# Kernel optimization log

Hardware: AMD Instinct MI355X
Metric: run time of the kernel (lower is better)

Reference implementation:

```python
import jax, jax.numpy as jnp
import numpy as np
import math

C = 512          # in_planes
H = 8            # num_heads
D = C // H       # head_dim = 64
EPS = 1e-12      # torch F.normalize eps


def _l2norm(x):
    # F.normalize(x, dim=-1): x / max(||x||_2, eps)
    n = jnp.sqrt(jnp.sum(x * x, axis=-1, keepdims=True))
    return x / jnp.maximum(n, EPS)


def setup_inputs() -> dict:
    key = jax.random.key(0)
    ks = jax.random.split(key, 8)
    q = jax.random.normal(ks[0], (8, 8, 256, C), dtype=jnp.float32)
    kv = jax.random.normal(ks[1], (8, 8, 512, C), dtype=jnp.float32)
    s = 0.02
    Wq = jax.random.normal(ks[2], (C, C), dtype=jnp.float32) * s
    bq = jax.random.normal(ks[3], (C,), dtype=jnp.float32) * s
    Wkv = jax.random.normal(ks[4], (2 * C, C), dtype=jnp.float32) * s
    bkv = jax.random.normal(ks[5], (2 * C,), dtype=jnp.float32) * s
    Wm = jax.random.normal(ks[6], (C, C), dtype=jnp.float32) * s
    bm = jax.random.normal(ks[7], (C,), dtype=jnp.float32) * s
    return {"q": q, "kv": kv, "Wq": Wq, "bq": bq, "Wkv": Wkv, "bkv": bkv, "Wm": Wm, "bm": bm}


def reference(q, kv, Wq, bq, Wkv, bkv, Wm, bm):
    b, t, lq, c = q.shape
    lk = kv.shape[2]
    shortcut = q

    # Q projection -> (b,t,h,lq,d), L2-normalized over d
    qh = (q @ Wq.T + bq).reshape(b, t, lq, H, D)
    qh = _l2norm(jnp.moveaxis(qh, 3, 2))  # (b,t,h,lq,d)

    # KV projection -> (b,t,2h,lk,d); first H heads = k, last H = v
    kvh = (kv @ Wkv.T + bkv).reshape(b, t, lk, 2 * H, D)
    kvh = jnp.moveaxis(kvh, 3, 2)          # (b,t,2h,lk,d)
    kh = _l2norm(kvh[:, :, :H])            # (b,t,h,lk,d)
    vh = _l2norm(kvh[:, :, H:])            # (b,t,h,lk,d)

    # cosine attention
    att = jnp.einsum('bthqd,bthkd->bthqk', qh, kh) / math.sqrt(D)
    att = jax.nn.softmax(att, axis=-1)
    x = jnp.einsum('bthqk,bthkd->bthqd', att, vh)  # (b,t,h,lq,d)

    # merge heads, output projection, residual
    x = jnp.moveaxis(x, 2, 3).reshape(b, t, lq, c)
    return x @ Wm.T + bm + shortcut
```

## Files before the change

### kernel.cpp

```cpp
#include <hip/hip_runtime.h>
#include <hip/hip_bf16.h>

using bf = __bf16;
typedef __attribute__((ext_vector_type(8))) __bf16 bf16x8;
typedef __attribute__((ext_vector_type(4))) float f32x4;

#define MFMA(a, b, c) __builtin_amdgcn_mfma_f32_16x16x32_bf16((a), (b), (c), 0, 0, 0)
#define GLL16(g, s)                                                         \
    __builtin_amdgcn_global_load_lds(                                       \
        (const __attribute__((address_space(1))) void*)(g),                 \
        (__attribute__((address_space(3))) void*)(s), 16, 0, 0)

static __device__ __forceinline__ void cvt_one(const float* __restrict__ s,
                                               bf* __restrict__ d, int i)
{
    const f32x4 a = ((const f32x4*)s)[2 * i];
    const f32x4 b = ((const f32x4*)s)[2 * i + 1];
    bf16x8 r;
#pragma unroll
    for (int k = 0; k < 4; ++k) { r[k] = (bf)a[k]; r[4 + k] = (bf)b[k]; }
    ((bf16x8*)d)[i] = r;
}

__global__ __launch_bounds__(256) void cvt2(const float* __restrict__ s1, bf* __restrict__ d1, int n1,
                                            const float* __restrict__ s2, bf* __restrict__ d2, int n2)
{
    int i = blockIdx.x * 256 + threadIdx.x;
    if (i < n1) { cvt_one(s1, d1, i); return; }
    i -= n1;
    if (i < n2) cvt_one(s2, d2, i);
}

__global__ __launch_bounds__(256) void cvt3(const float* __restrict__ s1, bf* __restrict__ d1, int n1,
                                            const float* __restrict__ s2, bf* __restrict__ d2, int n2,
                                            const float* __restrict__ s3, bf* __restrict__ d3, int n3)
{
    int i = blockIdx.x * 256 + threadIdx.x;
    if (i < n1) { cvt_one(s1, d1, i); return; }
    i -= n1;
    if (i < n2) { cvt_one(s2, d2, i); return; }
    i -= n2;
    if (i < n3) cvt_one(s3, d3, i);
}

template <int EPI>
__global__ __launch_bounds__(256) void gemm128(
    const bf* __restrict__ A, const bf* __restrict__ W,
    const float* __restrict__ bias, const float* __restrict__ res,
    void* __restrict__ Cout, int M, int N, int K)
{
    __shared__ __attribute__((aligned(16))) bf As[128 * 32];
    __shared__ __attribute__((aligned(16))) bf Bs[128 * 32];

    const int lane = threadIdx.x & 63;
    const int wave = threadIdx.x >> 6;
    const int lm = lane & 15;
    const int quad = lane >> 4;
    const int row0 = blockIdx.x * 128, col0 = blockIdx.y * 128;
    const int wrow = (wave >> 1) * 64, wcol = (wave & 1) * 64;

    const int sr = lane >> 2;
    const int sc = (lane & 3) * 8;
    const bf* Ag = A + (size_t)(row0 + wave * 32 + sr) * K + sc;
    const bf* Wg = W + (size_t)(col0 + wave * 32 + sr) * K + sc;
    bf* AsW = As + wave * 1024;
    bf* BsW = Bs + wave * 1024;

    f32x4 acc[4][4] = {};

    for (int k0 = 0; k0 < K; k0 += 32) {
        GLL16(Ag + k0, AsW);
        GLL16(Ag + (size_t)16 * K + k0, AsW + 512);
        GLL16(Wg + k0, BsW);
        GLL16(Wg + (size_t)16 * K + k0, BsW + 512);
        __syncthreads();

        bf16x8 a[4], b[4];
#pragma unroll
        for (int i = 0; i < 4; ++i)
            a[i] = *(const bf16x8*)(As + (wrow + i * 16 + lm) * 32 + quad * 8);
#pragma unroll
        for (int j = 0; j < 4; ++j)
            b[j] = *(const bf16x8*)(Bs + (wcol + j * 16 + lm) * 32 + quad * 8);
#pragma unroll
        for (int i = 0; i < 4; ++i)
#pragma unroll
            for (int j = 0; j < 4; ++j)
                acc[i][j] = MFMA(a[i], b[j], acc[i][j]);
        __syncthreads();
    }

    float bv[4];
#pragma unroll
    for (int j = 0; j < 4; ++j) bv[j] = bias[col0 + wcol + j * 16 + lm];

    if (EPI == 0) {
        bf* C = (bf*)Cout;
#pragma unroll
        for (int i = 0; i < 4; ++i) {
#pragma unroll
            for (int r = 0; r < 4; ++r) {
                float v[4];
                float ss = 0.f;
#pragma unroll
                for (int j = 0; j < 4; ++j) {
                    const float x = acc[i][j][r] + bv[j];
                    v[j] = x;
                    ss += x * x;
                }
                ss += __shfl_xor(ss, 1, 64);
                ss += __shfl_xor(ss, 2, 64);
                ss += __shfl_xor(ss, 4, 64);
                ss += __shfl_xor(ss, 8, 64);
                const float inv = 1.0f / fmaxf(sqrtf(ss), 1e-12f);
                const int row = row0 + wrow + i * 16 + quad * 4 + r;
#pragma unroll
                for (int j = 0; j < 4; ++j)
                    C[(size_t)row * N + col0 + wcol + j * 16 + lm] = (bf)(v[j] * inv);
            }
        }
    } else {
        float* C = (float*)Cout;
#pragma unroll
        for (int i = 0; i < 4; ++i) {
#pragma unroll
            for (int r = 0; r < 4; ++r) {
                const int row = row0 + wrow + i * 16 + quad * 4 + r;
#pragma unroll
                for (int j = 0; j < 4; ++j) {
                    const size_t idx = (size_t)row * N + col0 + wcol + j * 16 + lm;
                    C[idx] = acc[i][j][r] + bv[j] + res[idx];
                }
            }
        }
    }
}

__global__ __launch_bounds__(256, 4) void attn(
    const bf* __restrict__ qn, const bf* __restrict__ kvn, bf* __restrict__ X)
{
    __shared__ __attribute__((aligned(16))) bf Kt[128 * 72];
    __shared__ __attribute__((aligned(16))) bf Vt[64 * 136];
    __shared__ __attribute__((aligned(16))) bf Ps[4][16 * 40];

    const int qb = blockIdx.x >> 9;
    const int rb = blockIdx.x & 511;
    const int bt = rb >> 3;
    const int h = rb & 7;
    const int tid = threadIdx.x;
    const int lane = tid & 63;
    const int wave = tid >> 6;
    const int lm = lane & 15;
    const int quad = lane >> 4;

    const bf* qh = qn + ((size_t)bt * 256 + qb * 64) * 512 + h * 64;
    const bf* kh = kvn + (size_t)bt * 512 * 1024 + h * 64;
    const bf* vh = kh + 512;

    const bf* qp = qh + (size_t)(wave * 16 + lm) * 512 + quad * 8;
    const bf16x8 a0 = *(const bf16x8*)qp;
    const bf16x8 a1 = *(const bf16x8*)(qp + 32);

    f32x4 o[4] = {};
    float mrow[4] = {-1e30f, -1e30f, -1e30f, -1e30f};
    float lrow[4] = {};

    const int srow = tid >> 1;
    const int sseg = (tid & 1) * 32;

    for (int t = 0; t < 4; ++t) {
        {
            const bf* kr = kh + (size_t)(t * 128 + srow) * 1024 + sseg;
            bf* kd = Kt + srow * 72 + sseg;
#pragma unroll
            for (int j = 0; j < 4; ++j)
                *(bf16x8*)(kd + j * 8) = *(const bf16x8*)(kr + j * 8);

            const bf* vr = vh + (size_t)(t * 128 + srow) * 1024 + sseg;
            bf16x8 vv[4];
#pragma unroll
            for (int j = 0; j < 4; ++j) vv[j] = *(const bf16x8*)(vr + j * 8);
#pragma unroll
            for (int j = 0; j < 4; ++j)
#pragma unroll
                for (int e = 0; e < 8; ++e)
                    Vt[(sseg + j * 8 + e) * 136 + srow] = vv[j][e];
        }
        __syncthreads();

        f32x4 s[8];
#pragma unroll
        for (int nt = 0; nt < 8; ++nt) {
            const bf16x8 k0 = *(const bf16x8*)(&Kt[(nt * 16 + lm) * 72 + quad * 8]);
            const bf16x8 k1 = *(const bf16x8*)(&Kt[(nt * 16 + lm) * 72 + 32 + quad * 8]);
            f32x4 z = {};
            z = MFMA(a0, k0, z);
            s[nt] = MFMA(a1, k1, z);
        }

        float alpha[4], mnew[4];
#pragma unroll
        for (int rr = 0; rr < 4; ++rr) {
            float m = s[0][rr];
#pragma unroll
            for (int nt = 1; nt < 8; ++nt) m = fmaxf(m, s[nt][rr]);
            m = fmaxf(m, __shfl_xor(m, 1, 64));
            m = fmaxf(m, __shfl_xor(m, 2, 64));
            m = fmaxf(m, __shfl_xor(m, 4, 64));
            m = fmaxf(m, __shfl_xor(m, 8, 64));
            const float mn = fmaxf(mrow[rr], m);
            alpha[rr] = __expf((mrow[rr] - mn) * 0.125f);
            mnew[rr] = mn;
            mrow[rr] = mn;
        }
#pragma unroll
        for (int dt = 0; dt < 4; ++dt)
#pragma unroll
            for (int rr = 0; rr < 4; ++rr) o[dt][rr] *= alpha[rr];

        float tsum[4] = {};
        bf* Pw = &Ps[wave][0];
        for (int ntp = 0; ntp < 4; ++ntp) {
#pragma unroll
            for (int tt = 0; tt < 2; ++tt)
#pragma unroll
                for (int rr = 0; rr < 4; ++rr) {
                    const float e = __expf((s[ntp * 2 + tt][rr] - mnew[rr]) * 0.125f);
                    tsum[rr] += e;
                    Pw[(quad * 4 + rr) * 40 + tt * 16 + lm] = (bf)e;
                }
            const bf16x8 ap = *(const bf16x8*)(&Pw[lm * 40 + quad * 8]);
#pragma unroll
            for (int dt = 0; dt < 4; ++dt) {
                const bf16x8 bv = *(const bf16x8*)(&Vt[(dt * 16 + lm) * 136 + ntp * 32 + quad * 8]);
                o[dt] = MFMA(ap, bv, o[dt]);
            }
        }
#pragma unroll
        for (int rr = 0; rr < 4; ++rr) {
            float sm = tsum[rr];
            sm += __shfl_xor(sm, 1, 64);
            sm += __shfl_xor(sm, 2, 64);
            sm += __shfl_xor(sm, 4, 64);
            sm += __shfl_xor(sm, 8, 64);
            lrow[rr] = lrow[rr] * alpha[rr] + sm;
        }
        __syncthreads();
    }

    float inv[4];
#pragma unroll
    for (int rr = 0; rr < 4; ++rr) inv[rr] = 1.0f / lrow[rr];
    bf* Xp = X + ((size_t)bt * 256 + qb * 64 + wave * 16) * 512 + h * 64;
#pragma unroll
    for (int dt = 0; dt < 4; ++dt)
#pragma unroll
        for (int rr = 0; rr < 4; ++rr)
            Xp[(size_t)(quad * 4 + rr) * 512 + dt * 16 + lm] = (bf)(o[dt][rr] * inv[rr]);
}

extern "C" void kernel_launch(void* const* d_in, const int* in_sizes, int n_in,
                              void* d_out, int out_size, void* d_ws, size_t ws_size,
                              hipStream_t stream)
{
    const float* q   = (const float*)d_in[0];
    const float* kv  = (const float*)d_in[1];
    const float* Wq  = (const float*)d_in[2];
    const float* bq  = (const float*)d_in[3];
    const float* Wkv = (const float*)d_in[4];
    const float* bkv = (const float*)d_in[5];
    const float* Wm  = (const float*)d_in[6];
    const float* bm  = (const float*)d_in[7];
    float* out = (float*)d_out;

    char* ws = (char*)d_ws;
    bf* kvb = (bf*)ws;
    bf* kvn = (bf*)(ws + (size_t)(32 << 20));
    bf* wqb = (bf*)ws;
    bf* wmb = (bf*)(ws + (size_t)(16 << 20));
    bf* X   = (bf*)ws;
    char* dob = (char*)d_out;
    bf* wkvb = (bf*)dob;
    bf* qb   = (bf*)dob;
    bf* qn   = (bf*)(dob + (size_t)(16 << 20));

    cvt2<<<dim3(8448), 256, 0, stream>>>(kv, kvb, 2097152, Wkv, wkvb, 65536);
    gemm128<0><<<dim3(256, 8), 256, 0, stream>>>(kvb, wkvb, bkv, nullptr, kvn, 32768, 1024, 512);
    cvt3<<<dim3(4352), 256, 0, stream>>>(q, qb, 1048576, Wq, wqb, 32768, Wm, wmb, 32768);
    gemm128<0><<<dim3(128, 4), 256, 0, stream>>>(qb, wqb, bq, nullptr, qn, 16384, 512, 512);
    attn<<<dim3(2048), 256, 0, stream>>>(qn, kvn, X);
    gemm128<1><<<dim3(128, 4), 256, 0, stream>>>(X, wmb, bm, q, out, 16384, 512, 512);
}
```

Before: 306.8 us.

## Store projections head-major, drop online-softmax max, double query rows per block

The projection GEMM epilogues now write normalized Q/K/V in a head-major (bt, head, row, 64) layout, so attention reads contiguous 128-byte rows instead of strided 1024/2048-byte ones. The attention kernel drops the running max and rescaling of online softmax. Because inputs are L2-normalized, scores are bounded by 1 (times 1/8), so exp cannot overflow. Each block now handles 128 query rows (two 16-row chunks per wave), which halves the grid and the number of K/V tile loads, at the cost of more registers.

```diff
diff --git a/kernel.cpp b/kernel.cpp
--- a/kernel.cpp
+++ b/kernel.cpp
@@ -43,7 +43,7 @@
     if (i < n3) cvt_one(s3, d3, i);
 }
 
-template <int EPI>
+template <int EPI, int GH, int LGR>
 __global__ __launch_bounds__(256) void gemm128(
     const bf* __restrict__ A, const bf* __restrict__ W,
     const float* __restrict__ bias, const float* __restrict__ res,
@@ -96,15 +96,16 @@
 
     if (EPI == 0) {
         bf* C = (bf*)Cout;
+        const int g = (col0 + wcol) >> 6;
 #pragma unroll
         for (int i = 0; i < 4; ++i) {
 #pragma unroll
-            for (int r = 0; r < 4; ++r) {
+            for (int rg = 0; rg < 4; ++rg) {
                 float v[4];
                 float ss = 0.f;
 #pragma unroll
                 for (int j = 0; j < 4; ++j) {
-                    const float x = acc[i][j][r] + bv[j];
+                    const float x = acc[i][j][rg] + bv[j];
                     v[j] = x;
                     ss += x * x;
                 }
@@ -113,10 +114,13 @@
                 ss += __shfl_xor(ss, 4, 64);
                 ss += __shfl_xor(ss, 8, 64);
                 const float inv = 1.0f / fmaxf(sqrtf(ss), 1e-12f);
-                const int row = row0 + wrow + i * 16 + quad * 4 + r;
+                const int row = row0 + wrow + i * 16 + quad * 4 + rg;
+                const int bt = row >> LGR;
+                const int rl = row & ((1 << LGR) - 1);
+                bf* Cr = C + (((size_t)(bt * GH + g) << LGR) + rl) * 64;
 #pragma unroll
                 for (int j = 0; j < 4; ++j)
-                    C[(size_t)row * N + col0 + wcol + j * 16 + lm] = (bf)(v[j] * inv);
+                    Cr[j * 16 + lm] = (bf)(v[j] * inv);
             }
         }
     } else {
@@ -124,12 +128,12 @@
 #pragma unroll
         for (int i = 0; i < 4; ++i) {
 #pragma unroll
-            for (int r = 0; r < 4; ++r) {
-                const int row = row0 + wrow + i * 16 + quad * 4 + r;
+            for (int rg = 0; rg < 4; ++rg) {
+                const int row = row0 + wrow + i * 16 + quad * 4 + rg;
 #pragma unroll
                 for (int j = 0; j < 4; ++j) {
                     const size_t idx = (size_t)row * N + col0 + wcol + j * 16 + lm;
-                    C[idx] = acc[i][j][r] + bv[j] + res[idx];
+                    C[idx] = acc[i][j][rg] + bv[j] + res[idx];
                 }
             }
         }
@@ -153,30 +157,26 @@
     const int lm = lane & 15;
     const int quad = lane >> 4;
 
-    const bf* qh = qn + ((size_t)bt * 256 + qb * 64) * 512 + h * 64;
-    const bf* kh = kvn + (size_t)bt * 512 * 1024 + h * 64;
-    const bf* vh = kh + 512;
-
-    const bf* qp = qh + (size_t)(wave * 16 + lm) * 512 + quad * 8;
-    const bf16x8 a0 = *(const bf16x8*)qp;
-    const bf16x8 a1 = *(const bf16x8*)(qp + 32);
-
-    f32x4 o[4] = {};
-    float mrow[4] = {-1e30f, -1e30f, -1e30f, -1e30f};
-    float lrow[4] = {};
+    const bf* qh = qn + ((size_t)(bt * 8 + h) * 256 + qb * 128) * 64;
+    const bf* kh = kvn + (size_t)(bt * 16 + h) * 512 * 64;
+    const bf* vh = kvn + (size_t)(bt * 16 + 8 + h) * 512 * 64;
 
     const int srow = tid >> 1;
     const int sseg = (tid & 1) * 32;
 
+    f32x4 o[2][4] = {};
+    float sum[2][4] = {};
+    bf* Pw = &Ps[wave][0];
+
     for (int t = 0; t < 4; ++t) {
         {
-            const bf* kr = kh + (size_t)(t * 128 + srow) * 1024 + sseg;
+            const bf* kr = kh + (size_t)(t * 128 + srow) * 64 + sseg;
             bf* kd = Kt + srow * 72 + sseg;
 #pragma unroll
             for (int j = 0; j < 4; ++j)
                 *(bf16x8*)(kd + j * 8) = *(const bf16x8*)(kr + j * 8);
 
-            const bf* vr = vh + (size_t)(t * 128 + srow) * 1024 + sseg;
+            const bf* vr = vh + (size_t)(t * 128 + srow) * 64 + sseg;
             bf16x8 vv[4];
 #pragma unroll
             for (int j = 0; j < 4; ++j) vv[j] = *(const bf16x8*)(vr + j * 8);
@@ -188,75 +188,62 @@
         }
         __syncthreads();
 
-        f32x4 s[8];
-#pragma unroll
-        for (int nt = 0; nt < 8; ++nt) {
-            const bf16x8 k0 = *(const bf16x8*)(&Kt[(nt * 16 + lm) * 72 + quad * 8]);
-            const bf16x8 k1 = *(const bf16x8*)(&Kt[(nt * 16 + lm) * 72 + 32 + quad * 8]);
-            f32x4 z = {};
-            z = MFMA(a0, k0, z);
-            s[nt] = MFMA(a1, k1, z);
-        }
-
-        float alpha[4], mnew[4];
+#pragma unroll
+        for (int c = 0; c < 2; ++c) {
+            const int r0 = wave * 32 + c * 16;
+            const bf* qp = qh + (size_t)(r0 + lm) * 64 + quad * 8;
+            const bf16x8 a0 = *(const bf16x8*)qp;
+            const bf16x8 a1 = *(const bf16x8*)(qp + 32);
+
+            f32x4 s[8];
+#pragma unroll
+            for (int nt = 0; nt < 8; ++nt) {
+                const bf16x8 k0 = *(const bf16x8*)(&Kt[(nt * 16 + lm) * 72 + quad * 8]);
+                const bf16x8 k1 = *(const bf16x8*)(&Kt[(nt * 16 + lm) * 72 + 32 + quad * 8]);
+                f32x4 z = {};
+                z = MFMA(a0, k0, z);
+                s[nt] = MFMA(a1, k1, z);
+            }
+
+            for (int ntp = 0; ntp < 4; ++ntp) {
+#pragma unroll
+                for (int tt = 0; tt < 2; ++tt)
+#pragma unroll
+                    for (int rr = 0; rr < 4; ++rr) {
+                        const float e = __expf(s[ntp * 2 + tt][rr] * 0.125f);
+                        sum[c][rr] += e;
+                        Pw[(quad * 4 + rr) * 40 + tt * 16 + lm] = (bf)e;
+                    }
+                const bf16x8 ap = *(const bf16x8*)(&Pw[lm * 40 + quad * 8]);
+#pragma unroll
+                for (int dt = 0; dt < 4; ++dt) {
+                    const bf16x8 bv = *(const bf16x8*)(&Vt[(dt * 16 + lm) * 136 + ntp * 32 + quad * 8]);
+                    o[c][dt] = MFMA(ap, bv, o[c][dt]);
+                }
+            }
+        }
+        __syncthreads();
+    }
+
+#pragma unroll
+    for (int c = 0; c < 2; ++c) {
+        float inv[4];
 #pragma unroll
         for (int rr = 0; rr < 4; ++rr) {
-            float m = s[0][rr];
-#pragma unroll
-            for (int nt = 1; nt < 8; ++nt) m = fmaxf(m, s[nt][rr]);
-            m = fmaxf(m, __shfl_xor(m, 1, 64));
-            m = fmaxf(m, __shfl_xor(m, 2, 64));
-            m = fmaxf(m, __shfl_xor(m, 4, 64));
-            m = fmaxf(m, __shfl_xor(m, 8, 64));
-            const float mn = fmaxf(mrow[rr], m);
-            alpha[rr] = __expf((mrow[rr] - mn) * 0.125f);
-            mnew[rr] = mn;
-            mrow[rr] = mn;
-        }
-#pragma unroll
-        for (int dt = 0; dt < 4; ++dt)
-#pragma unroll
-            for (int rr = 0; rr < 4; ++rr) o[dt][rr] *= alpha[rr];
-
-        float tsum[4] = {};
-        bf* Pw = &Ps[wave][0];
-        for (int ntp = 0; ntp < 4; ++ntp) {
-#pragma unroll
-            for (int tt = 0; tt < 2; ++tt)
-#pragma unroll
-                for (int rr = 0; rr < 4; ++rr) {
-                    const float e = __expf((s[ntp * 2 + tt][rr] - mnew[rr]) * 0.125f);
-                    tsum[rr] += e;
-                    Pw[(quad * 4 + rr) * 40 + tt * 16 + lm] = (bf)e;
-                }
-            const bf16x8 ap = *(const bf16x8*)(&Pw[lm * 40 + quad * 8]);
-#pragma unroll
-            for (int dt = 0; dt < 4; ++dt) {
-                const bf16x8 bv = *(const bf16x8*)(&Vt[(dt * 16 + lm) * 136 + ntp * 32 + quad * 8]);
-                o[dt] = MFMA(ap, bv, o[dt]);
-            }
-        }
-#pragma unroll
-        for (int rr = 0; rr < 4; ++rr) {
-            float sm = tsum[rr];
+            float sm = sum[c][rr];
             sm += __shfl_xor(sm, 1, 64);
             sm += __shfl_xor(sm, 2, 64);
             sm += __shfl_xor(sm, 4, 64);
             sm += __shfl_xor(sm, 8, 64);
-            lrow[rr] = lrow[rr] * alpha[rr] + sm;
-        }
-        __syncthreads();
-    }
-
-    float inv[4];
-#pragma unroll
-    for (int rr = 0; rr < 4; ++rr) inv[rr] = 1.0f / lrow[rr];
-    bf* Xp = X + ((size_t)bt * 256 + qb * 64 + wave * 16) * 512 + h * 64;
-#pragma unroll
-    for (int dt = 0; dt < 4; ++dt)
-#pragma unroll
-        for (int rr = 0; rr < 4; ++rr)
-            Xp[(size_t)(quad * 4 + rr) * 512 + dt * 16 + lm] = (bf)(o[dt][rr] * inv[rr]);
+            inv[rr] = 1.0f / sm;
+        }
+        bf* Xp = X + ((size_t)bt * 256 + qb * 128 + wave * 32 + c * 16) * 512 + h * 64;
+#pragma unroll
+        for (int dt = 0; dt < 4; ++dt)
+#pragma unroll
+            for (int rr = 0; rr < 4; ++rr)
+                Xp[(size_t)(quad * 4 + rr) * 512 + dt * 16 + lm] = (bf)(o[c][dt][rr] * inv[rr]);
+    }
 }
 
 extern "C" void kernel_launch(void* const* d_in, const int* in_sizes, int n_in,
@@ -285,9 +272,9 @@
     bf* qn   = (bf*)(dob + (size_t)(16 << 20));
 
     cvt2<<<dim3(8448), 256, 0, stream>>>(kv, kvb, 2097152, Wkv, wkvb, 65536);
-    gemm128<0><<<dim3(256, 8), 256, 0, stream>>>(kvb, wkvb, bkv, nullptr, kvn, 32768, 1024, 512);
+    gemm128<0, 16, 9><<<dim3(256, 8), 256, 0, stream>>>(kvb, wkvb, bkv, nullptr, kvn, 32768, 1024, 512);
     cvt3<<<dim3(4352), 256, 0, stream>>>(q, qb, 1048576, Wq, wqb, 32768, Wm, wmb, 32768);
-    gemm128<0><<<dim3(128, 4), 256, 0, stream>>>(qb, wqb, bq, nullptr, qn, 16384, 512, 512);
-    attn<<<dim3(2048), 256, 0, stream>>>(qn, kvn, X);
-    gemm128<1><<<dim3(128, 4), 256, 0, stream>>>(X, wmb, bm, q, out, 16384, 512, 512);
-}
+    gemm128<0, 8, 8><<<dim3(128, 4), 256, 0, stream>>>(qb, wqb, bq, nullptr, qn, 16384, 512, 512);
+    attn<<<dim3(1024), 256, 0, stream>>>(qn, kvn, X);
+    gemm128<1, 0, 0><<<dim3(128, 4), 256, 0, stream>>>(X, wmb, bm, q, out, 16384, 512, 512);
+}
```

Result: faster. 282.8 us (-7.8%).
